# Performance work log

Hardware: AMD Instinct MI355X
Metric: run time of the kernel (lower is better)

Reference implementation:

```python
import jax, jax.numpy as jnp
import numpy as np

B, C, H, W = 16, 512, 64, 64


def setup_inputs() -> dict:
    key = jax.random.key(0)
    k1, k2 = jax.random.split(key)
    img_feat = jax.random.normal(k1, (B, C, H, W), dtype=jnp.float32)
    text_feat = jax.random.normal(k2, (B, C, H, W), dtype=jnp.float32)
    gamma = jnp.zeros((1,), dtype=jnp.float32)
    return {"img_feat": img_feat, "text_feat": text_feat, "gamma": gamma}


def reference(img_feat, text_feat, gamma):
    b, c, h, w = img_feat.shape
    q = img_feat.reshape(b, c, h * w)          # [B, C, HW]
    kv = text_feat.reshape(b, c, h * w)        # [B, C, HW]
    # channel-attention map: [B, C, C]
    attn = jnp.einsum('bcn,bdn->bcd', q, kv)
    attn = jax.nn.softmax(attn, axis=-1)
    info = jnp.einsum('bcd,bdn->bcn', attn, kv).reshape(b, c, h, w)
    return gamma * info + img_feat
```

## Files before the change

### kernel.cpp

```cpp
#include <hip/hip_runtime.h>
#include <hip/hip_bf16.h>


constexpr int NB = 16;
constexpr int NC = 512;
constexpr int NHW = 4096;
constexpr int QKSPLIT = 2;

typedef float f32x4 __attribute__((ext_vector_type(4)));
typedef __bf16 bf16x4 __attribute__((ext_vector_type(4)));
typedef __bf16 bf16x8 __attribute__((ext_vector_type(8)));

__device__ __forceinline__ void gload16(const void* g, void* l) {
  __builtin_amdgcn_global_load_lds(
      (const __attribute__((address_space(1))) void*)g,
      (__attribute__((address_space(3))) void*)l, 16, 0, 0);
}

template <int SPLITS>
__global__ __launch_bounds__(512) void gemm_qk(const float* __restrict__ Af,
                                               const __bf16* __restrict__ B,
                                               float* __restrict__ Dp) {
  __shared__ __bf16 sA[2][128 * 64];
  __shared__ __bf16 sB[2][128 * 64];

  const int t = threadIdx.x;
  const int lane = t & 63;
  const int wave = t >> 6;
  const int wr = wave >> 2;
  const int wc = wave & 3;

  constexpr int NWG = 16 * NB * SPLITS;
  constexpr int QX = NWG / 8;
  int flat = blockIdx.x + 4 * (blockIdx.y + 4 * blockIdx.z);
  flat = (flat & 7) * QX + (flat >> 3);
  const int bx = flat & 3;
  const int by = (flat >> 2) & 3;
  const int bz = flat >> 4;
  const int batch = bz / SPLITS;
  const int split = bz % SPLITS;

  const int aRow0 = bx * 128;
  const int bRow0 = by * 128;
  constexpr int KSUB = NHW / SPLITS;
  constexpr int NT = KSUB / 64;
  const int kBeg = split * KSUB;

  const int rl = lane >> 3;
  const int csrc = ((lane & 7) ^ rl) * 8;
  const __bf16* Bbase = B + (long)batch * NC * NHW +
                        (long)(bRow0 + wave * 16 + rl) * NHW + csrc + kBeg;
  const int ldsOff = wave * 16 * 64;

  const int c4 = (t & 15) * 4;
  const int rb = t >> 4;
  const float* Abase =
      Af + (long)batch * NC * NHW + (long)(aRow0 + rb) * NHW + kBeg + c4;

  f32x4 ra[4];
  auto loadA = [&](int kof) {
#pragma unroll
    for (int i = 0; i < 4; ++i)
      ra[i] = *(const f32x4*)(Abase + kof + (long)(32 * i) * NHW);
  };
  auto writeA = [&](int buf) {
#pragma unroll
    for (int i = 0; i < 4; ++i) {
      const int r = rb + 32 * i;
      const int idx = r * 64 + (c4 ^ ((r & 7) << 3));
      bf16x4 h = {(__bf16)ra[i].x, (__bf16)ra[i].y, (__bf16)ra[i].z,
                  (__bf16)ra[i].w};
      *(bf16x4*)&sA[buf][idx] = h;
    }
  };
  auto stageB = [&](int buf, int kof) {
#pragma unroll
    for (int i = 0; i < 2; ++i)
      gload16(Bbase + kof + (long)(i * 8) * NHW,
              &sB[buf][ldsOff + i * 8 * 64]);
  };

  f32x4 acc[4][2] = {};
  auto compute_tile = [&](int buf) {
#pragma unroll
    for (int kk = 0; kk < 2; ++kk) {
      const int kb = kk * 32 + ((lane >> 4) << 3);
      bf16x8 af[4], bfr[2];
#pragma unroll
      for (int m = 0; m < 4; ++m) {
        const int r = wr * 64 + m * 16 + (lane & 15);
        af[m] = *(const bf16x8*)&sA[buf][r * 64 + (kb ^ ((r & 7) << 3))];
      }
#pragma unroll
      for (int n = 0; n < 2; ++n) {
        const int r = wc * 32 + n * 16 + (lane & 15);
        bfr[n] = *(const bf16x8*)&sB[buf][r * 64 + (kb ^ ((r & 7) << 3))];
      }
#pragma unroll
      for (int m = 0; m < 4; ++m)
#pragma unroll
        for (int n = 0; n < 2; ++n)
          acc[m][n] = __builtin_amdgcn_mfma_f32_16x16x32_bf16(
              af[m], bfr[n], acc[m][n], 0, 0, 0);
    }
  };

  stageB(0, 0);
  loadA(0);
  asm volatile("s_waitcnt vmcnt(0)" ::: "memory");
  writeA(0);
  __syncthreads();

  int cur = 0;
#pragma unroll 1
  for (int tt = 0; tt < NT; ++tt) {
    const bool more = (tt + 1) < NT;
    if (more) {
      stageB(cur ^ 1, (tt + 1) * 64);
      loadA((tt + 1) * 64);
      asm volatile("" ::: "memory");
    }
    compute_tile(cur);
    if (more) {
      __builtin_amdgcn_s_barrier();
      asm volatile("s_waitcnt vmcnt(0)" ::: "memory");
      writeA(cur ^ 1);
      asm volatile("s_waitcnt lgkmcnt(0)" ::: "memory");
      __builtin_amdgcn_s_barrier();
      cur ^= 1;
    }
  }

  float* D = Dp + ((long)split * NB + batch) * NC * NC;
  const int m0 = aRow0 + wr * 64;
  const int n0 = bRow0 + wc * 32;
#pragma unroll
  for (int m = 0; m < 4; ++m)
#pragma unroll
    for (int n = 0; n < 2; ++n) {
      const int row0 = m0 + m * 16 + ((lane >> 4) << 2);
      const int col = n0 + n * 16 + (lane & 15);
#pragma unroll
      for (int r = 0; r < 4; ++r)
        D[(long)(row0 + r) * NC + col] = acc[m][n][r];
    }
}

__global__ __launch_bounds__(512) void gemm_pv(const __bf16* __restrict__ A,
                                               const __bf16* __restrict__ B,
                                               const float* __restrict__ img,
                                               const float* __restrict__ gammap,
                                               float* __restrict__ outp) {
  __shared__ __bf16 sA[128 * 64];
  __shared__ __bf16 sB[128 * 64];

  const int t = threadIdx.x;
  const int lane = t & 63;
  const int wave = t >> 6;
  const int wr = wave >> 2;
  const int wc = wave & 3;

  constexpr int GX = NHW / 128;
  constexpr int NWG = GX * 4 * NB;
  constexpr int QX = NWG / 8;
  int flat = blockIdx.x + GX * (blockIdx.y + 4 * blockIdx.z);
  flat = (flat & 7) * QX + (flat >> 3);
  const int bx = flat % GX;
  const int by = (flat / GX) & 3;
  const int batch = flat / (GX * 4);

  const int aRow0 = bx * 128;
  const int bRow0 = by * 128;

  const int rl = lane >> 3;
  const int csrc = ((lane & 7) ^ rl) * 8;
  const __bf16* Abase =
      A + (long)batch * NHW * NC + (long)(aRow0 + wave * 16 + rl) * NC + csrc;
  const __bf16* Bbase =
      B + (long)batch * NC * NC + (long)(bRow0 + wave * 16 + rl) * NC + csrc;
  const int ldsOff = wave * 16 * 64;

  f32x4 acc[4][2] = {};

#pragma unroll 1
  for (int k0 = 0; k0 < NC; k0 += 64) {
#pragma unroll
    for (int i = 0; i < 2; ++i) {
      gload16(Abase + k0 + (long)(i * 8) * NC, &sA[ldsOff + i * 8 * 64]);
      gload16(Bbase + k0 + (long)(i * 8) * NC, &sB[ldsOff + i * 8 * 64]);
    }
    __syncthreads();
#pragma unroll
    for (int kk = 0; kk < 2; ++kk) {
      const int kb = kk * 32 + ((lane >> 4) << 3);
      bf16x8 af[4], bfr[2];
#pragma unroll
      for (int m = 0; m < 4; ++m) {
        const int r = wr * 64 + m * 16 + (lane & 15);
        af[m] = *(const bf16x8*)&sA[r * 64 + (kb ^ ((r & 7) << 3))];
      }
#pragma unroll
      for (int n = 0; n < 2; ++n) {
        const int r = wc * 32 + n * 16 + (lane & 15);
        bfr[n] = *(const bf16x8*)&sB[r * 64 + (kb ^ ((r & 7) << 3))];
      }
#pragma unroll
      for (int m = 0; m < 4; ++m)
#pragma unroll
        for (int n = 0; n < 2; ++n)
          acc[m][n] = __builtin_amdgcn_mfma_f32_16x16x32_bf16(
              af[m], bfr[n], acc[m][n], 0, 0, 0);
    }
    __syncthreads();
  }

  const float g = gammap[0];
  const long obase = (long)batch * NC * NHW;
  const int sp0 = aRow0 + wr * 64;
  const int ch0 = bRow0 + wc * 32;
#pragma unroll
  for (int m = 0; m < 4; ++m)
#pragma unroll
    for (int n = 0; n < 2; ++n) {
      const int sp = sp0 + m * 16 + ((lane >> 4) << 2);
      const int ch = ch0 + n * 16 + (lane & 15);
      const long idx = obase + (long)ch * NHW + sp;
      f32x4 iv = *(const f32x4*)(img + idx);
      f32x4 ov;
#pragma unroll
      for (int r = 0; r < 4; ++r) ov[r] = g * acc[m][n][r] + iv[r];
      *(f32x4*)(outp + idx) = ov;
    }
}

__global__ __launch_bounds__(256) void prep_kv(const float* __restrict__ kv,
                                               __bf16* __restrict__ kv16,
                                               __bf16* __restrict__ kvT) {
  __shared__ __bf16 tile[64 * 68];
  const int t = threadIdx.x;
  const int n0 = blockIdx.x * 64;
  const int d0 = blockIdx.y * 64;
  const long ibase = (long)blockIdx.z * NC * NHW;

  const int nc4 = (t & 15) * 4;
  const int dr0 = t >> 4;
#pragma unroll
  for (int i = 0; i < 4; ++i) {
    const int dr = dr0 + 16 * i;
    f32x4 v = *(const f32x4*)(kv + ibase + (long)(d0 + dr) * NHW + n0 + nc4);
    bf16x4 h = {(__bf16)v.x, (__bf16)v.y, (__bf16)v.z, (__bf16)v.w};
    *(bf16x4*)&tile[dr * 68 + nc4] = h;
    *(bf16x4*)(kv16 + ibase + (long)(d0 + dr) * NHW + n0 + nc4) = h;
  }
  __syncthreads();

  const long obase = (long)blockIdx.z * NHW * NC;
  const int nr = t >> 2;
  const int dc0 = t & 3;
#pragma unroll
  for (int i = 0; i < 2; ++i) {
    const int dc = dc0 + 4 * i;
    bf16x8 pk;
#pragma unroll
    for (int j = 0; j < 8; ++j) pk[j] = tile[(dc * 8 + j) * 68 + nr];
    *(bf16x8*)(kvT + obase + (long)(n0 + nr) * NC + d0 + dc * 8) = pk;
  }
}

template <int SPLITS>
__global__ __launch_bounds__(256) void softmax_rows(
    const float* __restrict__ attn, __bf16* __restrict__ P) {
  const int row = blockIdx.x * 4 + (threadIdx.x >> 6);
  const int lane = threadIdx.x & 63;
  const long PS = (long)NB * NC * NC;
  const float* src = attn + (long)row * NC;

  float x[8] = {0.f, 0.f, 0.f, 0.f, 0.f, 0.f, 0.f, 0.f};
#pragma unroll
  for (int s = 0; s < SPLITS; ++s) {
    f32x4 v0 = *(const f32x4*)(src + s * PS + lane * 4);
    f32x4 v1 = *(const f32x4*)(src + s * PS + 256 + lane * 4);
#pragma unroll
    for (int r = 0; r < 4; ++r) { x[r] += v0[r]; x[4 + r] += v1[r]; }
  }

  float mx = x[0];
#pragma unroll
  for (int r = 1; r < 8; ++r) mx = fmaxf(mx, x[r]);
#pragma unroll
  for (int off = 32; off >= 1; off >>= 1) mx = fmaxf(mx, __shfl_xor(mx, off));

  float e[8], s = 0.f;
#pragma unroll
  for (int r = 0; r < 8; ++r) { e[r] = expf(x[r] - mx); s += e[r]; }
#pragma unroll
  for (int off = 32; off >= 1; off >>= 1) s += __shfl_xor(s, off);
  const float inv = 1.0f / s;

  __bf16* dst = P + (long)row * NC;
  bf16x4 h0, h1;
#pragma unroll
  for (int r = 0; r < 4; ++r) {
    h0[r] = (__bf16)(e[r] * inv);
    h1[r] = (__bf16)(e[4 + r] * inv);
  }
  *(bf16x4*)(dst + lane * 4) = h0;
  *(bf16x4*)(dst + 256 + lane * 4) = h1;
}

extern "C" void kernel_launch(void* const* d_in, const int* in_sizes, int n_in,
                              void* d_out, int out_size, void* d_ws,
                              size_t ws_size, hipStream_t stream) {
  const float* img = (const float*)d_in[0];
  const float* txt = (const float*)d_in[1];
  const float* gamma = (const float*)d_in[2];
  float* out = (float*)d_out;

  const size_t MiB = 1024 * 1024;
  __bf16* kv16 = (__bf16*)d_out;
  float* attnP = (float*)((char*)d_out + 68 * MiB);
  __bf16* kvT = (__bf16*)d_ws;
  __bf16* P = (__bf16*)((char*)d_ws + 64 * MiB);

  prep_kv<<<dim3(NHW / 64, NC / 64, NB), 256, 0, stream>>>(txt, kv16, kvT);

  gemm_qk<QKSPLIT><<<dim3(4, 4, NB * QKSPLIT), 512, 0, stream>>>(
      img, kv16, attnP);

  softmax_rows<QKSPLIT><<<dim3(NB * NC / 4), 256, 0, stream>>>(attnP, P);

  gemm_pv<<<dim3(NHW / 128, 4, NB), 512, 0, stream>>>(kvT, P, img, gamma, out);
}
```

Before: 216.1 us.

## Deepen QK GEMM prefetch to two tiles and prefetch residual in PV loop

```diff
diff --git a/kernel.cpp b/kernel.cpp
--- a/kernel.cpp
+++ b/kernel.cpp
@@ -22,7 +22,7 @@
                                                const __bf16* __restrict__ B,
                                                float* __restrict__ Dp) {
   __shared__ __bf16 sA[2][128 * 64];
-  __shared__ __bf16 sB[2][128 * 64];
+  __shared__ __bf16 sB[3][128 * 64];
 
   const int t = threadIdx.x;
   const int lane = t & 63;
@@ -57,13 +57,12 @@
   const float* Abase =
       Af + (long)batch * NC * NHW + (long)(aRow0 + rb) * NHW + kBeg + c4;
 
-  f32x4 ra[4];
-  auto loadA = [&](int kof) {
+  auto loadA = [&](f32x4 (&ra)[4], int kof) {
 #pragma unroll
     for (int i = 0; i < 4; ++i)
       ra[i] = *(const f32x4*)(Abase + kof + (long)(32 * i) * NHW);
   };
-  auto writeA = [&](int buf) {
+  auto writeA = [&](int buf, const f32x4 (&ra)[4]) {
 #pragma unroll
     for (int i = 0; i < 4; ++i) {
       const int r = rb + 32 * i;
@@ -76,12 +75,11 @@
   auto stageB = [&](int buf, int kof) {
 #pragma unroll
     for (int i = 0; i < 2; ++i)
-      gload16(Bbase + kof + (long)(i * 8) * NHW,
-              &sB[buf][ldsOff + i * 8 * 64]);
+      gload16(Bbase + kof + (long)(i * 8) * NHW, &sB[buf][ldsOff + i * 8 * 64]);
   };
 
   f32x4 acc[4][2] = {};
-  auto compute_tile = [&](int buf) {
+  auto compute_tile = [&](int bufA, int bufB) {
 #pragma unroll
     for (int kk = 0; kk < 2; ++kk) {
       const int kb = kk * 32 + ((lane >> 4) << 3);
@@ -89,12 +87,12 @@
 #pragma unroll
       for (int m = 0; m < 4; ++m) {
         const int r = wr * 64 + m * 16 + (lane & 15);
-        af[m] = *(const bf16x8*)&sA[buf][r * 64 + (kb ^ ((r & 7) << 3))];
+        af[m] = *(const bf16x8*)&sA[bufA][r * 64 + (kb ^ ((r & 7) << 3))];
       }
 #pragma unroll
       for (int n = 0; n < 2; ++n) {
         const int r = wc * 32 + n * 16 + (lane & 15);
-        bfr[n] = *(const bf16x8*)&sB[buf][r * 64 + (kb ^ ((r & 7) << 3))];
+        bfr[n] = *(const bf16x8*)&sB[bufB][r * 64 + (kb ^ ((r & 7) << 3))];
       }
 #pragma unroll
       for (int m = 0; m < 4; ++m)
@@ -105,30 +103,39 @@
     }
   };
 
+  f32x4 raE[4], raO[4];
+
+  loadA(raE, 0);
   stageB(0, 0);
-  loadA(0);
-  asm volatile("s_waitcnt vmcnt(0)" ::: "memory");
-  writeA(0);
-  __syncthreads();
-
-  int cur = 0;
-#pragma unroll 1
-  for (int tt = 0; tt < NT; ++tt) {
-    const bool more = (tt + 1) < NT;
-    if (more) {
-      stageB(cur ^ 1, (tt + 1) * 64);
-      loadA((tt + 1) * 64);
-      asm volatile("" ::: "memory");
-    }
-    compute_tile(cur);
-    if (more) {
-      __builtin_amdgcn_s_barrier();
-      asm volatile("s_waitcnt vmcnt(0)" ::: "memory");
-      writeA(cur ^ 1);
+  loadA(raO, 64);
+  stageB(1, 64);
+  asm volatile("s_waitcnt vmcnt(6)" ::: "memory");
+  writeA(0, raE);
+  asm volatile("s_waitcnt lgkmcnt(0)" ::: "memory");
+  __builtin_amdgcn_s_barrier();
+
+  auto body = [&](int tt, f32x4 (&raNext)[4], const f32x4 (&raCur)[4]) {
+    const bool deep = (tt + 2) < NT;
+    if (deep) {
+      loadA(raNext, (tt + 2) * 64);
+      stageB((tt + 2) % 3, (tt + 2) * 64);
+    }
+    compute_tile(tt & 1, tt % 3);
+    __builtin_amdgcn_s_barrier();
+    if (tt + 1 < NT) {
+      if (deep)
+        asm volatile("s_waitcnt vmcnt(6)" ::: "memory");
+      else
+        asm volatile("s_waitcnt vmcnt(0)" ::: "memory");
+      writeA((tt + 1) & 1, raCur);
       asm volatile("s_waitcnt lgkmcnt(0)" ::: "memory");
       __builtin_amdgcn_s_barrier();
-      cur ^= 1;
-    }
+    }
+  };
+#pragma unroll 1
+  for (int d = 0; d < NT / 2; ++d) {
+    body(2 * d, raE, raO);
+    body(2 * d + 1, raO, raE);
   }
 
   float* D = Dp + ((long)split * NB + batch) * NC * NC;
@@ -180,14 +187,26 @@
       B + (long)batch * NC * NC + (long)(bRow0 + wave * 16 + rl) * NC + csrc;
   const int ldsOff = wave * 16 * 64;
 
+  const long obase = (long)batch * NC * NHW;
+  const int sp0 = aRow0 + wr * 64;
+  const int ch0 = bRow0 + wc * 32;
+
   f32x4 acc[4][2] = {};
-
-#pragma unroll 1
-  for (int k0 = 0; k0 < NC; k0 += 64) {
+  f32x4 iv[8];
+
+#pragma unroll
+  for (int step = 0; step < 8; ++step) {
+    const int k0 = step * 64;
 #pragma unroll
     for (int i = 0; i < 2; ++i) {
       gload16(Abase + k0 + (long)(i * 8) * NC, &sA[ldsOff + i * 8 * 64]);
       gload16(Bbase + k0 + (long)(i * 8) * NC, &sB[ldsOff + i * 8 * 64]);
+    }
+    {
+      const int m = step >> 1, n = step & 1;
+      const int sp = sp0 + m * 16 + ((lane >> 4) << 2);
+      const int ch = ch0 + n * 16 + (lane & 15);
+      iv[step] = *(const f32x4*)(img + obase + (long)ch * NHW + sp);
     }
     __syncthreads();
 #pragma unroll
@@ -215,9 +234,6 @@
   }
 
   const float g = gammap[0];
-  const long obase = (long)batch * NC * NHW;
-  const int sp0 = aRow0 + wr * 64;
-  const int ch0 = bRow0 + wc * 32;
 #pragma unroll
   for (int m = 0; m < 4; ++m)
 #pragma unroll
@@ -225,10 +241,9 @@
       const int sp = sp0 + m * 16 + ((lane >> 4) << 2);
       const int ch = ch0 + n * 16 + (lane & 15);
       const long idx = obase + (long)ch * NHW + sp;
-      f32x4 iv = *(const f32x4*)(img + idx);
       f32x4 ov;
 #pragma unroll
-      for (int r = 0; r < 4; ++r) ov[r] = g * acc[m][n][r] + iv[r];
+      for (int r = 0; r < 4; ++r) ov[r] = g * acc[m][n][r] + iv[m * 2 + n][r];
       *(f32x4*)(outp + idx) = ov;
     }
 }
```

After: 228.9 us. 5.9% more time.

## Read fp32 text features directly in QK GEMM, drop bf16 copy

Applied to the files above, without the earlier changes.

```diff
diff --git a/kernel.cpp b/kernel.cpp
--- a/kernel.cpp
+++ b/kernel.cpp
@@ -19,7 +19,7 @@
 
 template <int SPLITS>
 __global__ __launch_bounds__(512) void gemm_qk(const float* __restrict__ Af,
-                                               const __bf16* __restrict__ B,
+                                               const float* __restrict__ Bf,
                                                float* __restrict__ Dp) {
   __shared__ __bf16 sA[2][128 * 64];
   __shared__ __bf16 sB[2][128 * 64];
@@ -46,22 +46,23 @@
   constexpr int NT = KSUB / 64;
   const int kBeg = split * KSUB;
 
-  const int rl = lane >> 3;
-  const int csrc = ((lane & 7) ^ rl) * 8;
-  const __bf16* Bbase = B + (long)batch * NC * NHW +
-                        (long)(bRow0 + wave * 16 + rl) * NHW + csrc + kBeg;
-  const int ldsOff = wave * 16 * 64;
-
   const int c4 = (t & 15) * 4;
   const int rb = t >> 4;
   const float* Abase =
       Af + (long)batch * NC * NHW + (long)(aRow0 + rb) * NHW + kBeg + c4;
-
-  f32x4 ra[4];
+  const float* Bbase =
+      Bf + (long)batch * NC * NHW + (long)(bRow0 + rb) * NHW + kBeg + c4;
+
+  f32x4 ra[4], rbv[4];
   auto loadA = [&](int kof) {
 #pragma unroll
     for (int i = 0; i < 4; ++i)
       ra[i] = *(const f32x4*)(Abase + kof + (long)(32 * i) * NHW);
+  };
+  auto loadB = [&](int kof) {
+#pragma unroll
+    for (int i = 0; i < 4; ++i)
+      rbv[i] = *(const f32x4*)(Bbase + kof + (long)(32 * i) * NHW);
   };
   auto writeA = [&](int buf) {
 #pragma unroll
@@ -73,11 +74,15 @@
       *(bf16x4*)&sA[buf][idx] = h;
     }
   };
-  auto stageB = [&](int buf, int kof) {
-#pragma unroll
-    for (int i = 0; i < 2; ++i)
-      gload16(Bbase + kof + (long)(i * 8) * NHW,
-              &sB[buf][ldsOff + i * 8 * 64]);
+  auto writeB = [&](int buf) {
+#pragma unroll
+    for (int i = 0; i < 4; ++i) {
+      const int r = rb + 32 * i;
+      const int idx = r * 64 + (c4 ^ ((r & 7) << 3));
+      bf16x4 h = {(__bf16)rbv[i].x, (__bf16)rbv[i].y, (__bf16)rbv[i].z,
+                  (__bf16)rbv[i].w};
+      *(bf16x4*)&sB[buf][idx] = h;
+    }
   };
 
   f32x4 acc[4][2] = {};
@@ -105,26 +110,30 @@
     }
   };
 
-  stageB(0, 0);
   loadA(0);
+  loadB(0);
+  asm volatile("s_waitcnt vmcnt(4)" ::: "memory");
+  writeA(0);
   asm volatile("s_waitcnt vmcnt(0)" ::: "memory");
-  writeA(0);
-  __syncthreads();
+  writeB(0);
+  asm volatile("s_waitcnt lgkmcnt(0)" ::: "memory");
+  __builtin_amdgcn_s_barrier();
 
   int cur = 0;
 #pragma unroll 1
   for (int tt = 0; tt < NT; ++tt) {
     const bool more = (tt + 1) < NT;
     if (more) {
-      stageB(cur ^ 1, (tt + 1) * 64);
       loadA((tt + 1) * 64);
+      loadB((tt + 1) * 64);
       asm volatile("" ::: "memory");
     }
     compute_tile(cur);
     if (more) {
-      __builtin_amdgcn_s_barrier();
+      asm volatile("s_waitcnt vmcnt(4)" ::: "memory");
+      writeA(cur ^ 1);
       asm volatile("s_waitcnt vmcnt(0)" ::: "memory");
-      writeA(cur ^ 1);
+      writeB(cur ^ 1);
       asm volatile("s_waitcnt lgkmcnt(0)" ::: "memory");
       __builtin_amdgcn_s_barrier();
       cur ^= 1;
@@ -234,7 +243,6 @@
 }
 
 __global__ __launch_bounds__(256) void prep_kv(const float* __restrict__ kv,
-                                               __bf16* __restrict__ kv16,
                                                __bf16* __restrict__ kvT) {
   __shared__ __bf16 tile[64 * 68];
   const int t = threadIdx.x;
@@ -250,7 +258,6 @@
     f32x4 v = *(const f32x4*)(kv + ibase + (long)(d0 + dr) * NHW + n0 + nc4);
     bf16x4 h = {(__bf16)v.x, (__bf16)v.y, (__bf16)v.z, (__bf16)v.w};
     *(bf16x4*)&tile[dr * 68 + nc4] = h;
-    *(bf16x4*)(kv16 + ibase + (long)(d0 + dr) * NHW + n0 + nc4) = h;
   }
   __syncthreads();
 
@@ -292,7 +299,7 @@
 
   float e[8], s = 0.f;
 #pragma unroll
-  for (int r = 0; r < 8; ++r) { e[r] = expf(x[r] - mx); s += e[r]; }
+  for (int r = 0; r < 8; ++r) { e[r] = __expf(x[r] - mx); s += e[r]; }
 #pragma unroll
   for (int off = 32; off >= 1; off >>= 1) s += __shfl_xor(s, off);
   const float inv = 1.0f / s;
@@ -317,15 +324,14 @@
   float* out = (float*)d_out;
 
   const size_t MiB = 1024 * 1024;
-  __bf16* kv16 = (__bf16*)d_out;
-  float* attnP = (float*)((char*)d_out + 68 * MiB);
+  float* attnP = (float*)d_out;
   __bf16* kvT = (__bf16*)d_ws;
   __bf16* P = (__bf16*)((char*)d_ws + 64 * MiB);
 
-  prep_kv<<<dim3(NHW / 64, NC / 64, NB), 256, 0, stream>>>(txt, kv16, kvT);
+  prep_kv<<<dim3(NHW / 64, NC / 64, NB), 256, 0, stream>>>(txt, kvT);
 
   gemm_qk<QKSPLIT><<<dim3(4, 4, NB * QKSPLIT), 512, 0, stream>>>(
-      img, kv16, attnP);
+      img, txt, attnP);
 
   softmax_rows<QKSPLIT><<<dim3(NB * NC / 4), 256, 0, stream>>>(attnP, P);
 
```

New measurement: 227.4 us. +5.2%, slower.

## Split QK reduction four ways, drop LDS double buffering, use fast exp

Applied to the files above, without the earlier changes.

```diff
diff --git a/kernel.cpp b/kernel.cpp
--- a/kernel.cpp
+++ b/kernel.cpp
@@ -5,7 +5,7 @@
 constexpr int NB = 16;
 constexpr int NC = 512;
 constexpr int NHW = 4096;
-constexpr int QKSPLIT = 2;
+constexpr int QKSPLIT = 4;
 
 typedef float f32x4 __attribute__((ext_vector_type(4)));
 typedef __bf16 bf16x4 __attribute__((ext_vector_type(4)));
@@ -21,8 +21,8 @@
 __global__ __launch_bounds__(512) void gemm_qk(const float* __restrict__ Af,
                                                const __bf16* __restrict__ B,
                                                float* __restrict__ Dp) {
-  __shared__ __bf16 sA[2][128 * 64];
-  __shared__ __bf16 sB[2][128 * 64];
+  __shared__ __bf16 sA[128 * 64];
+  __shared__ __bf16 sB[128 * 64];
 
   const int t = threadIdx.x;
   const int lane = t & 63;
@@ -58,30 +58,27 @@
       Af + (long)batch * NC * NHW + (long)(aRow0 + rb) * NHW + kBeg + c4;
 
   f32x4 ra[4];
-  auto loadA = [&](int kof) {
+  f32x4 acc[4][2] = {};
+
+#pragma unroll 1
+  for (int tt = 0; tt < NT; ++tt) {
+    const int kof = tt * 64;
 #pragma unroll
     for (int i = 0; i < 4; ++i)
       ra[i] = *(const f32x4*)(Abase + kof + (long)(32 * i) * NHW);
-  };
-  auto writeA = [&](int buf) {
+#pragma unroll
+    for (int i = 0; i < 2; ++i)
+      gload16(Bbase + kof + (long)(i * 8) * NHW, &sB[ldsOff + i * 8 * 64]);
+    asm volatile("s_waitcnt vmcnt(2)" ::: "memory");
 #pragma unroll
     for (int i = 0; i < 4; ++i) {
       const int r = rb + 32 * i;
       const int idx = r * 64 + (c4 ^ ((r & 7) << 3));
       bf16x4 h = {(__bf16)ra[i].x, (__bf16)ra[i].y, (__bf16)ra[i].z,
                   (__bf16)ra[i].w};
-      *(bf16x4*)&sA[buf][idx] = h;
-    }
-  };
-  auto stageB = [&](int buf, int kof) {
-#pragma unroll
-    for (int i = 0; i < 2; ++i)
-      gload16(Bbase + kof + (long)(i * 8) * NHW,
-              &sB[buf][ldsOff + i * 8 * 64]);
-  };
-
-  f32x4 acc[4][2] = {};
-  auto compute_tile = [&](int buf) {
+      *(bf16x4*)&sA[idx] = h;
+    }
+    __syncthreads();
 #pragma unroll
     for (int kk = 0; kk < 2; ++kk) {
       const int kb = kk * 32 + ((lane >> 4) << 3);
@@ -89,12 +86,12 @@
 #pragma unroll
       for (int m = 0; m < 4; ++m) {
         const int r = wr * 64 + m * 16 + (lane & 15);
-        af[m] = *(const bf16x8*)&sA[buf][r * 64 + (kb ^ ((r & 7) << 3))];
+        af[m] = *(const bf16x8*)&sA[r * 64 + (kb ^ ((r & 7) << 3))];
       }
 #pragma unroll
       for (int n = 0; n < 2; ++n) {
         const int r = wc * 32 + n * 16 + (lane & 15);
-        bfr[n] = *(const bf16x8*)&sB[buf][r * 64 + (kb ^ ((r & 7) << 3))];
+        bfr[n] = *(const bf16x8*)&sB[r * 64 + (kb ^ ((r & 7) << 3))];
       }
 #pragma unroll
       for (int m = 0; m < 4; ++m)
@@ -103,32 +100,7 @@
           acc[m][n] = __builtin_amdgcn_mfma_f32_16x16x32_bf16(
               af[m], bfr[n], acc[m][n], 0, 0, 0);
     }
-  };
-
-  stageB(0, 0);
-  loadA(0);
-  asm volatile("s_waitcnt vmcnt(0)" ::: "memory");
-  writeA(0);
-  __syncthreads();
-
-  int cur = 0;
-#pragma unroll 1
-  for (int tt = 0; tt < NT; ++tt) {
-    const bool more = (tt + 1) < NT;
-    if (more) {
-      stageB(cur ^ 1, (tt + 1) * 64);
-      loadA((tt + 1) * 64);
-      asm volatile("" ::: "memory");
-    }
-    compute_tile(cur);
-    if (more) {
-      __builtin_amdgcn_s_barrier();
-      asm volatile("s_waitcnt vmcnt(0)" ::: "memory");
-      writeA(cur ^ 1);
-      asm volatile("s_waitcnt lgkmcnt(0)" ::: "memory");
-      __builtin_amdgcn_s_barrier();
-      cur ^= 1;
-    }
+    __syncthreads();
   }
 
   float* D = Dp + ((long)split * NB + batch) * NC * NC;
@@ -292,7 +264,7 @@
 
   float e[8], s = 0.f;
 #pragma unroll
-  for (int r = 0; r < 8; ++r) { e[r] = expf(x[r] - mx); s += e[r]; }
+  for (int r = 0; r < 8; ++r) { e[r] = __expf(x[r] - mx); s += e[r]; }
 #pragma unroll
   for (int off = 32; off >= 1; off >>= 1) s += __shfl_xor(s, off);
   const float inv = 1.0f / s;
@@ -318,7 +290,7 @@
 
   const size_t MiB = 1024 * 1024;
   __bf16* kv16 = (__bf16*)d_out;
-  float* attnP = (float*)((char*)d_out + 68 * MiB);
+  float* attnP = (float*)((char*)d_out + 64 * MiB);
   __bf16* kvT = (__bf16*)d_ws;
   __bf16* P = (__bf16*)((char*)d_ws + 64 * MiB);
 
```

After: 241.5 us. 1.12x slower.
